# Optimization experiments

Hardware: AMD Instinct MI355X
Metric: run time of the kernel (lower is better)

Reference implementation:

```python
import jax, jax.numpy as jnp
import numpy as np

B, T, D, H = 2, 1024, 1024, 16
HS = D // H
EPS = 1e-5
SCALE = float(np.sqrt(HS))  # faithful bug: scores / hs**(-0.5) == scores * sqrt(hs)


def setup_inputs() -> dict:
    key = jax.random.key(0)
    ks = jax.random.split(key, 20)
    n = lambda k, shape: jax.random.normal(k, shape, dtype=jnp.float32) * 0.02
    return {
        "src": jax.random.normal(ks[0], (B, T, D), dtype=jnp.float32),
        "att": jax.random.normal(ks[1], (B, T, D), dtype=jnp.float32),
        # causal masked self-attention (no biases on q/k/v)
        "wq_m": n(ks[2], (H, D, HS)), "wk_m": n(ks[3], (H, D, HS)), "wv_m": n(ks[4], (H, D, HS)),
        "proj_m_w": n(ks[5], (D, D)), "proj_m_b": jnp.zeros((D,), jnp.float32),
        # final (cross) attention (biases on q/k/v)
        "wq_f": n(ks[6], (H, D, HS)), "wk_f": n(ks[7], (H, D, HS)), "wv_f": n(ks[8], (H, D, HS)),
        "bq_f": jnp.zeros((H, HS), jnp.float32), "bk_f": jnp.zeros((H, HS), jnp.float32),
        "bv_f": jnp.zeros((H, HS), jnp.float32),
        "proj_f_w": n(ks[9], (D, D)), "proj_f_b": jnp.zeros((D,), jnp.float32),
        # FFN
        "w1": n(ks[10], (D, 4 * D)), "b1": jnp.zeros((4 * D,), jnp.float32),
        "w2": n(ks[11], (4 * D, D)), "b2": jnp.zeros((D,), jnp.float32),
        # shared RMSNorm weight (one instance reused at all three sites)
        "norm_w": jnp.ones((D,), jnp.float32),
    }


def rmsnorm(x, w):
    return x * jax.lax.rsqrt(jnp.mean(x * x, axis=-1, keepdims=True) + EPS) * w


def masked_attn(x, wq, wk, wv):
    q = jnp.einsum('btd,hde->bhte', x, wq)
    k = jnp.einsum('btd,hde->bhte', x, wk)
    v = jnp.einsum('btd,hde->bhte', x, wv)
    scores = jnp.einsum('bhte,bhse->bhts', q, k) * SCALE  # [B,H,T,T]
    causal = jnp.tril(jnp.ones((T, T), dtype=bool))
    scores = jnp.where(causal, scores, -jnp.inf)
    a = jax.nn.softmax(scores, axis=-1)
    o = jnp.einsum('bhts,bhse->bhte', a, v)
    return o.transpose(0, 2, 1, 3).reshape(B, T, D)  # concat heads


def final_attn(x, att, wq, bq, wk, bk, wv, bv):
    q = jnp.einsum('btd,hde->bhte', att, wq) + bq[None, :, None, :]
    k = jnp.einsum('btd,hde->bhte', att, wk) + bk[None, :, None, :]
    v = jnp.einsum('btd,hde->bhte', x, wv) + bv[None, :, None, :]
    scores = jnp.einsum('bhte,bhse->bhts', q, k) * SCALE
    a = jax.nn.softmax(scores, axis=-1)
    o = jnp.einsum('bhts,bhse->bhte', a, v)
    return o.transpose(0, 2, 1, 3).reshape(B, T, D)


def reference(src, att, wq_m, wk_m, wv_m, proj_m_w, proj_m_b,
              wq_f, wk_f, wv_f, bq_f, bk_f, bv_f, proj_f_w, proj_f_b,
              w1, b1, w2, b2, norm_w):
    # masked self-attention block
    m = masked_attn(rmsnorm(src, norm_w), wq_m, wk_m, wv_m)
    m_out = src + (m @ proj_m_w + proj_m_b)
    # cross attention block (q/k from norm(att), v from m_out)
    f = final_attn(m_out, rmsnorm(att, norm_w), wq_f, bq_f, wk_f, bk_f, wv_f, bv_f)
    f_out = m_out + (f @ proj_f_w + proj_f_b)
    # FFN block
    h = rmsnorm(f_out, norm_w)
    h = jax.nn.gelu(h @ w1 + b1, approximate=False) @ w2 + b2
    return f_out + h
```

## Files before the change

### kernel.cpp

```cpp
#include <hip/hip_runtime.h>
#include <math.h>

#define BB 2
#define TT 1024
#define DD 1024
#define HH 16
#define HS 64
#define NROWS (BB*TT)

typedef _Float16 f16;
typedef __attribute__((ext_vector_type(8))) _Float16 half8;
typedef __attribute__((ext_vector_type(4))) _Float16 half4;
typedef __attribute__((ext_vector_type(4))) float f32x4;

constexpr float EPS   = 1e-5f;
constexpr float SCALE = 8.0f;

__device__ __forceinline__ void load_lds16(const f16* g, f16* l) {
    __builtin_amdgcn_global_load_lds(
        (const __attribute__((address_space(1))) unsigned int*)g,
        (__attribute__((address_space(3))) unsigned int*)l, 16, 0, 0);
}

__device__ __forceinline__ int xcd_swizzle(int lin, int total) {
    if ((total & 7) == 0) {
        const int chunk = total >> 3;
        lin = (lin & 7) * chunk + (lin >> 3);
    }
    return lin;
}

__global__ __launch_bounds__(256) void rms2_kernel(const float* __restrict__ src,
                                                   const float* __restrict__ att,
                                                   const float* __restrict__ w,
                                                   f16* __restrict__ xn_s,
                                                   f16* __restrict__ xn_a) {
    const int bid = blockIdx.x;
    const int tid = threadIdx.x;
    const int row = bid & (NROWS - 1);
    const float* xr = ((bid < NROWS) ? src : att) + (size_t)row * DD;
    f16* out = ((bid < NROWS) ? xn_s : xn_a) + (size_t)row * DD;

    float4 xv = reinterpret_cast<const float4*>(xr)[tid];
    float ss = xv.x*xv.x + xv.y*xv.y + xv.z*xv.z + xv.w*xv.w;

    __shared__ float red[256];
    red[tid] = ss; __syncthreads();
    for (int s = 128; s > 0; s >>= 1) {
        if (tid < s) red[tid] += red[tid + s];
        __syncthreads();
    }
    const float inv = rsqrtf(red[0] * (1.0f / DD) + EPS);

    float4 wv = reinterpret_cast<const float4*>(w)[tid];
    half4 o;
    o.x = (f16)(xv.x * inv * wv.x);
    o.y = (f16)(xv.y * inv * wv.y);
    o.z = (f16)(xv.z * inv * wv.z);
    o.w = (f16)(xv.w * inv * wv.w);
    *reinterpret_cast<half4*>(&out[tid * 4]) = o;
}

__global__ __launch_bounds__(256) void wtrans_all(
    const float* __restrict__ wq_m, const float* __restrict__ wk_m,
    const float* __restrict__ wv_m, const float* __restrict__ proj_m_w,
    const float* __restrict__ wq_f, const float* __restrict__ wk_f,
    const float* __restrict__ wv_f, const float* __restrict__ proj_f_w,
    const float* __restrict__ w1,   const float* __restrict__ w2,
    f16* __restrict__ wt,
    const float* __restrict__ bq, const float* __restrict__ bk,
    float* __restrict__ biascat)
{
    const int bid = blockIdx.x;
    const int tid = threadIdx.x;
    const size_t M_ = 1024 * 1024;

    if (bid >= 4096) {
        for (int j = tid; j < 5120; j += 256)
            biascat[j] = (j < 3072) ? 0.f : ((j < 4096) ? bq[j - 3072] : bk[j - 4096]);
        return;
    }

    const float* W; f16* Wt; int K, N, lognk, t; bool headw;
    if (bid < 768)       { const int m = bid >> 8;
                           W = (m == 0) ? wq_m : (m == 1) ? wk_m : wv_m;
                           Wt = wt + (size_t)m * M_;
                           K = 1024; N = 1024; lognk = 4; headw = true;  t = bid & 255; }
    else if (bid < 1024) { W = proj_m_w; Wt = wt + 6 * M_;
                           K = 1024; N = 1024; lognk = 4; headw = false; t = bid - 768; }
    else if (bid < 1792) { const int m = (bid - 1024) >> 8;
                           W = (m == 0) ? wq_f : (m == 1) ? wk_f : wv_f;
                           Wt = wt + (size_t)(3 + m) * M_;
                           K = 1024; N = 1024; lognk = 4; headw = true;  t = (bid - 1024) & 255; }
    else if (bid < 2048) { W = proj_f_w; Wt = wt + 7 * M_;
                           K = 1024; N = 1024; lognk = 4; headw = false; t = bid - 1792; }
    else if (bid < 3072) { W = w1; Wt = wt + 8 * M_;
                           K = 1024; N = 4096; lognk = 4; headw = false; t = bid - 2048; }
    else                 { W = w2; Wt = wt + 12 * M_;
                           K = 4096; N = 1024; lognk = 6; headw = false; t = bid - 3072; }

    const int k0 = (t & ((1 << lognk) - 1)) * 64;
    const int n0 = (t >> lognk) * 64;

    __shared__ float tt[64][65];
    #pragma unroll
    for (int r = 0; r < 4; ++r) {
        const int idx = tid + r * 256;
        const int kl  = idx >> 4;
        const int nl4 = (idx & 15) * 4;
        const float* gp;
        if (headw) {
            gp = W + ((size_t)(n0 >> 6) * K + (k0 + kl)) * 64 + nl4;
        } else {
            gp = W + (size_t)(k0 + kl) * N + n0 + nl4;
        }
        float4 v = *reinterpret_cast<const float4*>(gp);
        tt[kl][nl4 + 0] = v.x; tt[kl][nl4 + 1] = v.y;
        tt[kl][nl4 + 2] = v.z; tt[kl][nl4 + 3] = v.w;
    }
    __syncthreads();
    #pragma unroll
    for (int r = 0; r < 4; ++r) {
        const int idx = tid + r * 256;
        const int nl  = idx >> 4;
        const int kl4 = (idx & 15) * 4;
        half4 o;
        o.x = (f16)tt[kl4 + 0][nl];
        o.y = (f16)tt[kl4 + 1][nl];
        o.z = (f16)tt[kl4 + 2][nl];
        o.w = (f16)tt[kl4 + 3][nl];
        *reinterpret_cast<half4*>(&Wt[(size_t)(n0 + nl) * K + k0 + kl4]) = o;
    }
}

template<int BM, int EPI, bool HEADOUT, bool SPLITA, bool OHALF, bool PARTIAL>
__global__ __launch_bounds__(256, 2) void gemm_mfma(
    const f16* __restrict__ A1,
    const f16* __restrict__ A2,
    const f16* __restrict__ Bt,
    const float* __restrict__ bias,
    float* __restrict__ outF,
    f16* __restrict__ outH,
    int N, int K, int splitN)
{
    constexpr int BK = 32;
    constexpr int MI = 4;
    constexpr int NI = (BM == 128) ? 4 : 2;
    constexpr int WN = (BM == 128) ? 64 : 32;
    constexpr int ASLOT = BM * 4;
    constexpr int AINST = ASLOT / 256;

    __shared__ f16 ldsA[2][ASLOT * 8];
    __shared__ f16 ldsB[2][512 * 8];

    const int tid  = threadIdx.x;
    const int lane = tid & 63;
    const int wid  = tid >> 6;
    const int gy = gridDim.y;
    const int lin = xcd_swizzle(blockIdx.y * gridDim.x + blockIdx.x,
                                gridDim.x * gy);
    const int m0 = (lin % gy) * BM;
    const int n0 = (lin / gy) * 128;
    const int wm = (BM == 128) ? (wid >> 1) : 0;
    const int wn = (BM == 128) ? (wid & 1) : wid;

    const int Klen  = K / gridDim.z;
    const int kbase = blockIdx.z * Klen;

    const f16* Aptr = (SPLITA && n0 >= splitN) ? A2 : A1;

    f32x4 acc[MI][NI];
    #pragma unroll
    for (int i = 0; i < MI; ++i)
        #pragma unroll
        for (int j = 0; j < NI; ++j)
            acc[i][j] = (f32x4){0.f, 0.f, 0.f, 0.f};

    auto stage = [&](int buf, int kt) {
        const int k0 = kbase + kt * BK;
        #pragma unroll
        for (int i = 0; i < AINST; ++i) {
            const int s   = (wid * AINST + i) * 64 + lane;
            const int kh  = s / BM;
            const int row = s % BM;
            load_lds16(Aptr + (size_t)(m0 + row) * K + (k0 + kh * 8),
                       &ldsA[buf][s * 8]);
        }
        #pragma unroll
        for (int i = 0; i < 2; ++i) {
            const int s   = (wid * 2 + i) * 64 + lane;
            const int kh  = s >> 7;
            const int col = s & 127;
            load_lds16(Bt + (size_t)(n0 + col) * K + (k0 + kh * 8),
                       &ldsB[buf][s * 8]);
        }
    };

    const int NT = Klen / BK;
    stage(0, 0);
    __syncthreads();
    int cur = 0;
    const int l15 = lane & 15, l4 = lane >> 4;
    for (int kt = 0; kt < NT; ++kt) {
        if (kt + 1 < NT) stage(cur ^ 1, kt + 1);
        half8 af[MI], bfr[NI];
        #pragma unroll
        for (int mi = 0; mi < MI; ++mi)
            af[mi] = *reinterpret_cast<const half8*>(
                &ldsA[cur][(l4 * BM + wm * 64 + mi * 16 + l15) * 8]);
        #pragma unroll
        for (int ni = 0; ni < NI; ++ni)
            bfr[ni] = *reinterpret_cast<const half8*>(
                &ldsB[cur][(l4 * 128 + wn * WN + ni * 16 + l15) * 8]);
        #pragma unroll
        for (int mi = 0; mi < MI; ++mi)
            #pragma unroll
            for (int ni = 0; ni < NI; ++ni)
                acc[mi][ni] = __builtin_amdgcn_mfma_f32_16x16x32_f16(
                    af[mi], bfr[ni], acc[mi][ni], 0, 0, 0);
        __syncthreads();
        cur ^= 1;
    }

    f16* pout = nullptr;
    if (PARTIAL) {
        const size_t MN = (size_t)gridDim.y * BM * N;
        pout = outH + (size_t)blockIdx.z * MN;
    }

    #pragma unroll
    for (int mi = 0; mi < MI; ++mi) {
        #pragma unroll
        for (int ni = 0; ni < NI; ++ni) {
            #pragma unroll
            for (int r = 0; r < 4; ++r) {
                const int row = m0 + wm * 64 + mi * 16 + l4 * 4 + r;
                const int col = n0 + wn * WN + ni * 16 + l15;
                float v = acc[mi][ni][r];
                if (PARTIAL) {
                    pout[(size_t)row * N + col] = (f16)v;
                    continue;
                }
                if (EPI >= 1) v += bias[col];
                if (EPI == 2) v = 0.5f * v * (1.0f + erff(v * 0.70710678118f));
                size_t oidx;
                if (HEADOUT) {
                    const int mat = col >> 10;
                    const int h = (col >> 6) & 15, e = col & 63;
                    const int b = row >> 10, t = row & (TT - 1);
                    oidx = (size_t)mat * ((size_t)NROWS * DD)
                         + ((size_t)((b * HH + h) * TT + t)) * HS + e;
                } else {
                    oidx = (size_t)row * N + col;
                }
                if (OHALF) outH[oidx] = (f16)v;
                else       outF[oidx] = v;
            }
        }
    }
}

template<int MODE>
__global__ __launch_bounds__(256) void reduce_fuse(const f16* __restrict__ part,
                                                   const float* __restrict__ bias,
                                                   const float* __restrict__ residF,
                                                   const f16* __restrict__ residH,
                                                   float* __restrict__ outF,
                                                   f16* __restrict__ outH,
                                                   const float* __restrict__ normw,
                                                   f16* __restrict__ xnout) {
    const size_t MN  = (size_t)NROWS * 1024;
    const int tid = threadIdx.x;
    const size_t idx = ((size_t)blockIdx.x * 256 + tid) * 4;
    float o[4];
    {
        half4 p0 = *reinterpret_cast<const half4*>(part + idx);
        half4 p1 = *reinterpret_cast<const half4*>(part + MN + idx);
        half4 p2 = *reinterpret_cast<const half4*>(part + 2 * MN + idx);
        half4 p3 = *reinterpret_cast<const half4*>(part + 3 * MN + idx);
        float4 bi = *reinterpret_cast<const float4*>(bias + (idx & 1023));
        o[0] = (float)p0.x + (float)p1.x + (float)p2.x + (float)p3.x + bi.x;
        o[1] = (float)p0.y + (float)p1.y + (float)p2.y + (float)p3.y + bi.y;
        o[2] = (float)p0.z + (float)p1.z + (float)p2.z + (float)p3.z + bi.z;
        o[3] = (float)p0.w + (float)p1.w + (float)p2.w + (float)p3.w + bi.w;
    }
    if (MODE == 0 || MODE == 2) {
        float4 rs = *reinterpret_cast<const float4*>(residF + idx);
        o[0] += rs.x; o[1] += rs.y; o[2] += rs.z; o[3] += rs.w;
    } else {
        half4 rh = *reinterpret_cast<const half4*>(residH + idx);
        o[0] += (float)rh.x; o[1] += (float)rh.y; o[2] += (float)rh.z; o[3] += (float)rh.w;
    }

    if (MODE == 0) {
        half4 h;
        h.x = (f16)o[0]; h.y = (f16)o[1]; h.z = (f16)o[2]; h.w = (f16)o[3];
        *reinterpret_cast<half4*>(outH + idx) = h;
        return;
    }

    float4 ov = {o[0], o[1], o[2], o[3]};
    *reinterpret_cast<float4*>(outF + idx) = ov;

    if (MODE == 1) {
        __shared__ float red[256];
        red[tid] = o[0]*o[0] + o[1]*o[1] + o[2]*o[2] + o[3]*o[3];
        __syncthreads();
        for (int s = 128; s > 0; s >>= 1) {
            if (tid < s) red[tid] += red[tid + s];
            __syncthreads();
        }
        const float inv = rsqrtf(red[0] * (1.0f / DD) + EPS);
        float4 nw = *reinterpret_cast<const float4*>(normw + (idx & 1023));
        half4 h;
        h.x = (f16)(o[0] * inv * nw.x);
        h.y = (f16)(o[1] * inv * nw.y);
        h.z = (f16)(o[2] * inv * nw.z);
        h.w = (f16)(o[3] * inv * nw.w);
        *reinterpret_cast<half4*>(xnout + idx) = h;
    }
}

template<bool CAUSAL>
__global__ __launch_bounds__(256) void attn_mfma(const f16* __restrict__ Q,
                                                 const f16* __restrict__ Kg,
                                                 const f16* __restrict__ Vg,
                                                 f16* __restrict__ O) {
    const int iq  = blockIdx.x;
    const int bh  = blockIdx.y;
    const int tid = threadIdx.x;
    const int lane = tid & 63;
    const int w   = tid >> 6;
    const int l15 = lane & 15, l4 = lane >> 4;

    __shared__ f16 Ks[512 * 8];
    __shared__ f16 VT[64 * 72];
    __shared__ f16 Ps[4][16 * 72];

    const f16* qb = Q  + ((size_t)bh * TT + (size_t)iq * 64) * HS;
    const f16* kb = Kg + (size_t)bh * TT * HS;
    const f16* vb = Vg + (size_t)bh * TT * HS;

    half8 qf[2];
    #pragma unroll
    for (int ks = 0; ks < 2; ++ks)
        qf[ks] = *reinterpret_cast<const half8*>(
            qb + (size_t)(w * 16 + l15) * HS + ks * 32 + l4 * 8);

    f32x4 oacc[4];
    #pragma unroll
    for (int ni = 0; ni < 4; ++ni) oacc[ni] = (f32x4){0.f, 0.f, 0.f, 0.f};
    float m_run[4], l_run[4];
    #pragma unroll
    for (int r = 0; r < 4; ++r) { m_run[r] = -1e30f; l_run[r] = 0.f; }

    const int sp  = lane & 31;
    const int ehv = lane >> 5;
    const int c0  = w * 16 + ehv * 8;

    const int ntiles = CAUSAL ? (iq + 1) : (TT / 64);
    for (int js = 0; js < ntiles; ++js) {
        __syncthreads();

        #pragma unroll
        for (int i = 0; i < 2; ++i) {
            const int slot = (w * 2 + i) * 64 + lane;
            load_lds16(kb + (size_t)(js * 64 + (slot & 63)) * HS + (slot >> 6) * 8,
                       &Ks[slot * 8]);
        }
        {
            const f16* vrow = vb + (size_t)(js * 64 + 2 * sp) * HS + c0;
            uint4 r0 = *reinterpret_cast<const uint4*>(vrow);
            uint4 r1 = *reinterpret_cast<const uint4*>(vrow + HS);
            const unsigned rc0[4] = {r0.x, r0.y, r0.z, r0.w};
            const unsigned rc1[4] = {r1.x, r1.y, r1.z, r1.w};
            #pragma unroll
            for (int i = 0; i < 8; ++i) {
                const unsigned lo = (i & 1) ? (rc0[i >> 1] >> 16) : (rc0[i >> 1] & 0xffffu);
                const unsigned hi = (i & 1) ? (rc1[i >> 1] >> 16) : (rc1[i >> 1] & 0xffffu);
                *reinterpret_cast<unsigned*>(&VT[(c0 + i) * 72 + 2 * sp]) = lo | (hi << 16);
            }
        }
        __syncthreads();

        f32x4 sacc[4];
        #pragma unroll
        for (int ni = 0; ni < 4; ++ni) sacc[ni] = (f32x4){0.f, 0.f, 0.f, 0.f};
        #pragma unroll
        for (int ks = 0; ks < 2; ++ks) {
            #pragma unroll
            for (int ni = 0; ni < 4; ++ni) {
                half8 kf = *reinterpret_cast<const half8*>(
                    &Ks[((ks * 4 + l4) * 64 + ni * 16 + l15) * 8]);
                sacc[ni] = __builtin_amdgcn_mfma_f32_16x16x32_f16(qf[ks], kf, sacc[ni], 0, 0, 0);
            }
        }

        float sv[4][4];
        #pragma unroll
        for (int ni = 0; ni < 4; ++ni) {
            #pragma unroll
            for (int r = 0; r < 4; ++r) {
                float x = sacc[ni][r] * SCALE;
                if (CAUSAL && js == iq) {
                    const int sg = js * 64 + ni * 16 + l15;
                    const int qg = iq * 64 + w * 16 + l4 * 4 + r;
                    if (sg > qg) x = -1e30f;
                }
                sv[ni][r] = x;
            }
        }

        #pragma unroll
        for (int r = 0; r < 4; ++r) {
            float rm = fmaxf(fmaxf(sv[0][r], sv[1][r]), fmaxf(sv[2][r], sv[3][r]));
            rm = fmaxf(rm, __shfl_xor(rm, 1));
            rm = fmaxf(rm, __shfl_xor(rm, 2));
            rm = fmaxf(rm, __shfl_xor(rm, 4));
            rm = fmaxf(rm, __shfl_xor(rm, 8));
            const float mnew = fmaxf(m_run[r], rm);
            const float corr = __expf(m_run[r] - mnew);
            float p0 = __expf(sv[0][r] - mnew);
            float p1 = __expf(sv[1][r] - mnew);
            float p2 = __expf(sv[2][r] - mnew);
            float p3 = __expf(sv[3][r] - mnew);
            float sum = p0 + p1 + p2 + p3;
            sum += __shfl_xor(sum, 1);
            sum += __shfl_xor(sum, 2);
            sum += __shfl_xor(sum, 4);
            sum += __shfl_xor(sum, 8);
            l_run[r] = l_run[r] * corr + sum;
            m_run[r] = mnew;
            #pragma unroll
            for (int ni = 0; ni < 4; ++ni) oacc[ni][r] *= corr;
            f16* prow = &Ps[w][(l4 * 4 + r) * 72];
            prow[ 0 + l15] = (f16)p0;
            prow[16 + l15] = (f16)p1;
            prow[32 + l15] = (f16)p2;
            prow[48 + l15] = (f16)p3;
        }

        #pragma unroll
        for (int ks = 0; ks < 2; ++ks) {
            half8 pf = *reinterpret_cast<const half8*>(&Ps[w][l15 * 72 + ks * 32 + l4 * 8]);
            #pragma unroll
            for (int ni = 0; ni < 4; ++ni) {
                half8 vf = *reinterpret_cast<const half8*>(
                    &VT[(ni * 16 + l15) * 72 + ks * 32 + l4 * 8]);
                oacc[ni] = __builtin_amdgcn_mfma_f32_16x16x32_f16(pf, vf, oacc[ni], 0, 0, 0);
            }
        }
    }

    const int b = bh >> 4, h = bh & (HH - 1);
    #pragma unroll
    for (int r = 0; r < 4; ++r) {
        const float inv = 1.0f / l_run[r];
        const int t = iq * 64 + w * 16 + l4 * 4 + r;
        #pragma unroll
        for (int ni = 0; ni < 4; ++ni)
            O[((size_t)(b * TT + t)) * DD + h * HS + ni * 16 + l15] =
                (f16)(oacc[ni][r] * inv);
    }
}

extern "C" void kernel_launch(void* const* d_in, const int* in_sizes, int n_in,
                              void* d_out, int out_size, void* d_ws, size_t ws_size,
                              hipStream_t stream) {
    const float* src      = (const float*)d_in[0];
    const float* att      = (const float*)d_in[1];
    const float* wq_m     = (const float*)d_in[2];
    const float* wk_m     = (const float*)d_in[3];
    const float* wv_m     = (const float*)d_in[4];
    const float* proj_m_w = (const float*)d_in[5];
    const float* proj_m_b = (const float*)d_in[6];
    const float* wq_f     = (const float*)d_in[7];
    const float* wk_f     = (const float*)d_in[8];
    const float* wv_f     = (const float*)d_in[9];
    const float* bq_f     = (const float*)d_in[10];
    const float* bk_f     = (const float*)d_in[11];
    const float* bv_f     = (const float*)d_in[12];
    const float* proj_f_w = (const float*)d_in[13];
    const float* proj_f_b = (const float*)d_in[14];
    const float* w1       = (const float*)d_in[15];
    const float* b1       = (const float*)d_in[16];
    const float* w2       = (const float*)d_in[17];
    const float* b2       = (const float*)d_in[18];
    const float* norm_w   = (const float*)d_in[19];

    const size_t M_ = 1024 * 1024;
    f16* wsb = (f16*)d_ws;
    f16* wt      = wsb;
    f16* headbuf = wsb + 16 * M_;
    f16* h1      = wsb + 16 * M_;
    f16* xn_s    = wsb + 28 * M_;
    f16* xn_a    = wsb + 30 * M_;
    f16* ao      = wsb + 32 * M_;
    f16* mo_h    = wsb + 34 * M_;
    f16* partH   = wsb + 36 * M_;
    float* biascat = (float*)d_out;
    float* f_out = (float*)d_out;
    float* outp  = (float*)d_out;
    (void)ws_size; (void)in_sizes; (void)n_in;

    const dim3 blk(256);
    const int BIG = 1 << 30;
    const dim3 gQKV(40, 16);
    const dim3 gVF(8, 32);
    const dim3 gW1(32, 16);
    const dim3 gSPLIT(8, 16, 4);
    const dim3 gRED(2048);

    wtrans_all<<<dim3(4097), blk, 0, stream>>>(
        wq_m, wk_m, wv_m, proj_m_w, wq_f, wk_f, wv_f, proj_f_w, w1, w2,
        wt, bq_f, bk_f, biascat);
    rms2_kernel<<<dim3(2 * NROWS), blk, 0, stream>>>(src, att, norm_w, xn_s, xn_a);

    gemm_mfma<128, 1, true, true, true, false><<<gQKV, blk, 0, stream>>>(
        xn_s, xn_a, wt, biascat, nullptr, headbuf, 5120, 1024, 3072);

    attn_mfma<true><<<dim3(16, 32), blk, 0, stream>>>(
        headbuf, headbuf + 2 * M_, headbuf + 4 * M_, ao);
    gemm_mfma<128, 0, false, false, false, true><<<gSPLIT, blk, 0, stream>>>(
        ao, nullptr, wt + 6 * M_, nullptr, nullptr, partH, 1024, 1024, BIG);
    reduce_fuse<0><<<gRED, blk, 0, stream>>>(
        partH, proj_m_b, src, nullptr, nullptr, mo_h, nullptr, nullptr);

    gemm_mfma<64, 1, true, false, true, false><<<gVF, blk, 0, stream>>>(
        mo_h, nullptr, wt + 5 * M_, bv_f, nullptr, headbuf + 10 * M_, 1024, 1024, BIG);
    attn_mfma<false><<<dim3(16, 32), blk, 0, stream>>>(
        headbuf + 6 * M_, headbuf + 8 * M_, headbuf + 10 * M_, ao);
    gemm_mfma<128, 0, false, false, false, true><<<gSPLIT, blk, 0, stream>>>(
        ao, nullptr, wt + 7 * M_, nullptr, nullptr, partH, 1024, 1024, BIG);
    reduce_fuse<1><<<gRED, blk, 0, stream>>>(
        partH, proj_f_b, nullptr, mo_h, f_out, nullptr, norm_w, xn_s);

    gemm_mfma<128, 2, false, false, true, false><<<gW1, blk, 0, stream>>>(
        xn_s, nullptr, wt + 8 * M_, b1, nullptr, h1, 4096, 1024, BIG);
    gemm_mfma<128, 0, false, false, false, true><<<gSPLIT, blk, 0, stream>>>(
        h1, nullptr, wt + 12 * M_, nullptr, nullptr, partH, 1024, 4096, BIG);
    reduce_fuse<2><<<gRED, blk, 0, stream>>>(
        partH, b2, f_out, nullptr, outp, nullptr, nullptr, nullptr);
}
```

Before: 312.2 us.

## Merge RMSNorm into weight-prologue, split-K W1 GEMM with GELU reduce, add MFMA priority hints

Folds the initial RMSNorm kernel into the weight transpose prologue to save one launch. Converts the W1 GEMM to a split-K=2 variant writing fp16 partials, then adds a separate kernel that sums them, applies bias and exact GELU. It also raises wave priority around MFMA sections in attention. The split-K path adds extra partial-sum memory traffic and a launch in exchange for more blocks in the W1 GEMM, and the fp16 partials may lose a little precision.

```diff
diff --git a/kernel.cpp b/kernel.cpp
--- a/kernel.cpp
+++ b/kernel.cpp
@@ -30,38 +30,7 @@
     return lin;
 }
 
-__global__ __launch_bounds__(256) void rms2_kernel(const float* __restrict__ src,
-                                                   const float* __restrict__ att,
-                                                   const float* __restrict__ w,
-                                                   f16* __restrict__ xn_s,
-                                                   f16* __restrict__ xn_a) {
-    const int bid = blockIdx.x;
-    const int tid = threadIdx.x;
-    const int row = bid & (NROWS - 1);
-    const float* xr = ((bid < NROWS) ? src : att) + (size_t)row * DD;
-    f16* out = ((bid < NROWS) ? xn_s : xn_a) + (size_t)row * DD;
-
-    float4 xv = reinterpret_cast<const float4*>(xr)[tid];
-    float ss = xv.x*xv.x + xv.y*xv.y + xv.z*xv.z + xv.w*xv.w;
-
-    __shared__ float red[256];
-    red[tid] = ss; __syncthreads();
-    for (int s = 128; s > 0; s >>= 1) {
-        if (tid < s) red[tid] += red[tid + s];
-        __syncthreads();
-    }
-    const float inv = rsqrtf(red[0] * (1.0f / DD) + EPS);
-
-    float4 wv = reinterpret_cast<const float4*>(w)[tid];
-    half4 o;
-    o.x = (f16)(xv.x * inv * wv.x);
-    o.y = (f16)(xv.y * inv * wv.y);
-    o.z = (f16)(xv.z * inv * wv.z);
-    o.w = (f16)(xv.w * inv * wv.w);
-    *reinterpret_cast<half4*>(&out[tid * 4]) = o;
-}
-
-__global__ __launch_bounds__(256) void wtrans_all(
+__global__ __launch_bounds__(256) void prologue_all(
     const float* __restrict__ wq_m, const float* __restrict__ wk_m,
     const float* __restrict__ wv_m, const float* __restrict__ proj_m_w,
     const float* __restrict__ wq_f, const float* __restrict__ wk_f,
@@ -69,15 +38,45 @@
     const float* __restrict__ w1,   const float* __restrict__ w2,
     f16* __restrict__ wt,
     const float* __restrict__ bq, const float* __restrict__ bk,
-    float* __restrict__ biascat)
+    float* __restrict__ biascat,
+    const float* __restrict__ src, const float* __restrict__ att,
+    const float* __restrict__ normw,
+    f16* __restrict__ xn_s, f16* __restrict__ xn_a)
 {
     const int bid = blockIdx.x;
     const int tid = threadIdx.x;
     const size_t M_ = 1024 * 1024;
 
-    if (bid >= 4096) {
+    __shared__ float tt[64][65];
+
+    if (bid == 4096) {
         for (int j = tid; j < 5120; j += 256)
             biascat[j] = (j < 3072) ? 0.f : ((j < 4096) ? bq[j - 3072] : bk[j - 4096]);
+        return;
+    }
+
+    if (bid > 4096) {
+        const int rrow = bid - 4097;
+        const int row  = rrow & (NROWS - 1);
+        const float* xr = ((rrow < NROWS) ? src : att) + (size_t)row * DD;
+        f16* out = ((rrow < NROWS) ? xn_s : xn_a) + (size_t)row * DD;
+
+        float4 xv = reinterpret_cast<const float4*>(xr)[tid];
+        float ss = xv.x*xv.x + xv.y*xv.y + xv.z*xv.z + xv.w*xv.w;
+        float* red = &tt[0][0];
+        red[tid] = ss; __syncthreads();
+        for (int s = 128; s > 0; s >>= 1) {
+            if (tid < s) red[tid] += red[tid + s];
+            __syncthreads();
+        }
+        const float inv = rsqrtf(red[0] * (1.0f / DD) + EPS);
+        float4 wv = reinterpret_cast<const float4*>(normw)[tid];
+        half4 o;
+        o.x = (f16)(xv.x * inv * wv.x);
+        o.y = (f16)(xv.y * inv * wv.y);
+        o.z = (f16)(xv.z * inv * wv.z);
+        o.w = (f16)(xv.w * inv * wv.w);
+        *reinterpret_cast<half4*>(&out[tid * 4]) = o;
         return;
     }
 
@@ -102,7 +101,6 @@
     const int k0 = (t & ((1 << lognk) - 1)) * 64;
     const int n0 = (t >> lognk) * 64;
 
-    __shared__ float tt[64][65];
     #pragma unroll
     for (int r = 0; r < 4; ++r) {
         const int idx = tid + r * 256;
@@ -321,6 +319,27 @@
     }
 }
 
+__global__ __launch_bounds__(256) void reduce_gelu(const f16* __restrict__ part,
+                                                   const float* __restrict__ b1,
+                                                   f16* __restrict__ h1out) {
+    const size_t MN  = (size_t)NROWS * 4096;
+    const size_t idx = ((size_t)blockIdx.x * 256 + threadIdx.x) * 4;
+    half4 p0 = *reinterpret_cast<const half4*>(part + idx);
+    half4 p1 = *reinterpret_cast<const half4*>(part + MN + idx);
+    float4 bi = *reinterpret_cast<const float4*>(b1 + (idx & 4095));
+    float o[4];
+    o[0] = (float)p0.x + (float)p1.x + bi.x;
+    o[1] = (float)p0.y + (float)p1.y + bi.y;
+    o[2] = (float)p0.z + (float)p1.z + bi.z;
+    o[3] = (float)p0.w + (float)p1.w + bi.w;
+    half4 h;
+    #pragma unroll
+    for (int j = 0; j < 4; ++j)
+        o[j] = 0.5f * o[j] * (1.0f + erff(o[j] * 0.70710678118f));
+    h.x = (f16)o[0]; h.y = (f16)o[1]; h.z = (f16)o[2]; h.w = (f16)o[3];
+    *reinterpret_cast<half4*>(h1out + idx) = h;
+}
+
 template<bool CAUSAL>
 __global__ __launch_bounds__(256) void attn_mfma(const f16* __restrict__ Q,
                                                  const f16* __restrict__ Kg,
@@ -386,6 +405,7 @@
         f32x4 sacc[4];
         #pragma unroll
         for (int ni = 0; ni < 4; ++ni) sacc[ni] = (f32x4){0.f, 0.f, 0.f, 0.f};
+        __builtin_amdgcn_s_setprio(1);
         #pragma unroll
         for (int ks = 0; ks < 2; ++ks) {
             #pragma unroll
@@ -395,6 +415,7 @@
                 sacc[ni] = __builtin_amdgcn_mfma_f32_16x16x32_f16(qf[ks], kf, sacc[ni], 0, 0, 0);
             }
         }
+        __builtin_amdgcn_s_setprio(0);
 
         float sv[4][4];
         #pragma unroll
@@ -440,6 +461,7 @@
             prow[48 + l15] = (f16)p3;
         }
 
+        __builtin_amdgcn_s_setprio(1);
         #pragma unroll
         for (int ks = 0; ks < 2; ++ks) {
             half8 pf = *reinterpret_cast<const half8*>(&Ps[w][l15 * 72 + ks * 32 + l4 * 8]);
@@ -450,6 +472,7 @@
                 oacc[ni] = __builtin_amdgcn_mfma_f32_16x16x32_f16(pf, vf, oacc[ni], 0, 0, 0);
             }
         }
+        __builtin_amdgcn_s_setprio(0);
     }
 
     const int b = bh >> 4, h = bh & (HH - 1);
@@ -498,6 +521,8 @@
     f16* ao      = wsb + 32 * M_;
     f16* mo_h    = wsb + 34 * M_;
     f16* partH   = wsb + 36 * M_;
+    f16* partW1  = wsb + 28 * M_;
+    f16* xn2     = wsb + 44 * M_;
     float* biascat = (float*)d_out;
     float* f_out = (float*)d_out;
     float* outp  = (float*)d_out;
@@ -507,14 +532,14 @@
     const int BIG = 1 << 30;
     const dim3 gQKV(40, 16);
     const dim3 gVF(8, 32);
-    const dim3 gW1(32, 16);
+    const dim3 gW1(32, 16, 2);
     const dim3 gSPLIT(8, 16, 4);
     const dim3 gRED(2048);
-
-    wtrans_all<<<dim3(4097), blk, 0, stream>>>(
+    const dim3 gREDW1(8192);
+
+    prologue_all<<<dim3(8193), blk, 0, stream>>>(
         wq_m, wk_m, wv_m, proj_m_w, wq_f, wk_f, wv_f, proj_f_w, w1, w2,
-        wt, bq_f, bk_f, biascat);
-    rms2_kernel<<<dim3(2 * NROWS), blk, 0, stream>>>(src, att, norm_w, xn_s, xn_a);
+        wt, bq_f, bk_f, biascat, src, att, norm_w, xn_s, xn_a);
 
     gemm_mfma<128, 1, true, true, true, false><<<gQKV, blk, 0, stream>>>(
         xn_s, xn_a, wt, biascat, nullptr, headbuf, 5120, 1024, 3072);
@@ -533,10 +558,11 @@
     gemm_mfma<128, 0, false, false, false, true><<<gSPLIT, blk, 0, stream>>>(
         ao, nullptr, wt + 7 * M_, nullptr, nullptr, partH, 1024, 1024, BIG);
     reduce_fuse<1><<<gRED, blk, 0, stream>>>(
-        partH, proj_f_b, nullptr, mo_h, f_out, nullptr, norm_w, xn_s);
-
-    gemm_mfma<128, 2, false, false, true, false><<<gW1, blk, 0, stream>>>(
-        xn_s, nullptr, wt + 8 * M_, b1, nullptr, h1, 4096, 1024, BIG);
+        partH, proj_f_b, nullptr, mo_h, f_out, nullptr, norm_w, xn2);
+
+    gemm_mfma<128, 0, false, false, false, true><<<gW1, blk, 0, stream>>>(
+        xn2, nullptr, wt + 8 * M_, nullptr, nullptr, partW1, 4096, 1024, BIG);
+    reduce_gelu<<<gREDW1, blk, 0, stream>>>(partW1, b1, h1);
     gemm_mfma<128, 0, false, false, false, true><<<gSPLIT, blk, 0, stream>>>(
         h1, nullptr, wt + 12 * M_, nullptr, nullptr, partH, 1024, 4096, BIG);
     reduce_fuse<2><<<gRED, blk, 0, stream>>>(
```

New measurement: 310.4 us. About the same (-0.6%).
